# Optimization experiments

Hardware: AMD Instinct MI355X
Metric: run time of the kernel (lower is better)

Reference implementation:

```python
import jax, jax.numpy as jnp
import numpy as np

N_SRC = 50000
N_DST = 50000
E = 1600000
IN_DIM = 128
OUT_DIM = 128
EDGE_DIM = 64
NUM_HEADS = 4
HEAD_DIM = OUT_DIM // NUM_HEADS


def setup_inputs() -> dict:
    key = jax.random.key(0)
    ks = jax.random.split(key, 10)
    return {
        "h_src": jax.random.normal(ks[0], (N_SRC, IN_DIM), dtype=jnp.float32),
        "h_dst": jax.random.normal(ks[1], (N_DST, IN_DIM), dtype=jnp.float32),
        "edge_feat": jax.random.normal(ks[2], (E, EDGE_DIM), dtype=jnp.float32),
        "edge_index": jnp.stack([
            jax.random.randint(ks[3], (E,), 0, N_SRC),
            jax.random.randint(ks[4], (E,), 0, N_DST),
        ], axis=0).astype(jnp.int64) if False else jnp.stack([
            jax.random.randint(ks[3], (E,), 0, N_SRC),
            jax.random.randint(ks[4], (E,), 0, N_DST),
        ], axis=0),
        # weights stored [in, out]; y = x @ W (same math as torch Linear with W^T)
        "W_src": jax.random.normal(ks[5], (IN_DIM, OUT_DIM), dtype=jnp.float32) * 0.05,
        "W_dst": jax.random.normal(ks[6], (IN_DIM, OUT_DIM), dtype=jnp.float32) * 0.05,
        "W_edge": jax.random.normal(ks[7], (EDGE_DIM, OUT_DIM), dtype=jnp.float32) * 0.05,
        "a_src": jax.random.normal(ks[8], (NUM_HEADS, HEAD_DIM), dtype=jnp.float32) * 0.1,
        "a_dst": jax.random.normal(ks[9], (NUM_HEADS, HEAD_DIM), dtype=jnp.float32) * 0.1,
        "a_edge": jax.random.normal(jax.random.fold_in(key, 10), (NUM_HEADS, HEAD_DIM), dtype=jnp.float32) * 0.1,
    }


def reference(h_src, h_dst, edge_feat, edge_index, W_src, W_dst, W_edge, a_src, a_dst, a_edge):
    num_dst = h_dst.shape[0]
    src_idx, dst_idx = edge_index[0], edge_index[1]

    hs = (h_src @ W_src).reshape(-1, NUM_HEADS, HEAD_DIM)   # [N_src, H, D]
    hd = (h_dst @ W_dst).reshape(-1, NUM_HEADS, HEAD_DIM)   # [N_dst, H, D]
    he = (edge_feat @ W_edge).reshape(-1, NUM_HEADS, HEAD_DIM)  # [E, H, D]

    # per-node attention logit components, gathered to edges
    e_src_n = jnp.einsum('nhd,hd->nh', hs, a_src)  # [N_src, H]
    e_dst_n = jnp.einsum('nhd,hd->nh', hd, a_dst)  # [N_dst, H]
    e_edge = jnp.einsum('ehd,hd->eh', he, a_edge)  # [E, H]
    e = e_src_n[src_idx] + e_dst_n[dst_idx] + e_edge  # [E, H]
    e = jnp.where(e > 0, e, 0.2 * e)  # leaky_relu(0.2)

    # segmented softmax over edges grouped by destination node
    e_max = jax.ops.segment_max(e, dst_idx, num_segments=num_dst)  # [N_dst, H]
    e_max = jnp.where(jnp.isfinite(e_max), e_max, 0.0)  # empty segments
    e_exp = jnp.exp(e - e_max[dst_idx])  # [E, H]
    e_sum = jax.ops.segment_sum(e_exp, dst_idx, num_segments=num_dst)  # [N_dst, H]
    alpha = e_exp / (e_sum[dst_idx] + 1e-8)  # [E, H]

    # weighted scatter-aggregate of source features
    msg = alpha[..., None] * hs[src_idx]  # [E, H, D]
    out = jax.ops.segment_sum(msg, dst_idx, num_segments=num_dst)  # [N_dst, H, D]
    return out.reshape(num_dst, NUM_HEADS * HEAD_DIM)
```

## Files before the change

### kernel.cpp

```cpp
#include <hip/hip_runtime.h>

typedef _Float16 half_t;

#define N_SRCN 50000
#define N_DSTN 50000
#define NE     1600000
#define IN_DIM 128
#define OUT_DIMN 128
#define EDGE_DIMN 64
#define NHEAD  4
#define HDIM   32


__global__ __launch_bounds__(512) void k_combine(
    const float* __restrict__ Wsrc, const float* __restrict__ Wdst,
    const float* __restrict__ Wedge,
    const float* __restrict__ asrc, const float* __restrict__ adst,
    const float* __restrict__ aedge,
    float* __restrict__ c_src, float* __restrict__ c_dst,
    float* __restrict__ c_edgeH) {
    int t = threadIdx.x;
    int k = t >> 2, h = t & 3;
    float s1 = 0.f, s2 = 0.f;
    #pragma unroll
    for (int d = 0; d < HDIM; ++d) {
        s1 += Wsrc[k * OUT_DIMN + h * HDIM + d] * asrc[h * HDIM + d];
        s2 += Wdst[k * OUT_DIMN + h * HDIM + d] * adst[h * HDIM + d];
    }
    c_src[t] = s1;
    c_dst[t] = s2;
    if (t < EDGE_DIMN * NHEAD) {
        float s3 = 0.f;
        #pragma unroll
        for (int d = 0; d < HDIM; ++d)
            s3 += Wedge[k * OUT_DIMN + h * HDIM + d] * aedge[h * HDIM + d];
        c_edgeH[h * EDGE_DIMN + k] = s3;
    }
}

__global__ __launch_bounds__(256) void k_node_logits(
    const float* __restrict__ X, const float* __restrict__ c,
    float* __restrict__ outl, int N) {
    int row = blockIdx.x * 4 + (threadIdx.x >> 6);
    int l = threadIdx.x & 63;
    if (row >= N) return;
    float x0 = X[(size_t)row * IN_DIM + l];
    float x1 = X[(size_t)row * IN_DIM + 64 + l];
    #pragma unroll
    for (int h = 0; h < NHEAD; ++h) {
        float s = x0 * c[l * 4 + h] + x1 * c[(64 + l) * 4 + h];
        #pragma unroll
        for (int off = 32; off; off >>= 1) s += __shfl_xor(s, off, 64);
        if (l == h) outl[(size_t)row * 4 + h] = s;
    }
}

__global__ __launch_bounds__(256) void k_hist(
    const int* __restrict__ dstI, int* __restrict__ counts) {
    int e = blockIdx.x * 256 + threadIdx.x;
    if (e < NE) atomicAdd(&counts[dstI[e]], 1);
}

__global__ __launch_bounds__(1024) void k_scan(
    const int* __restrict__ cnt, int* __restrict__ offs, int* __restrict__ cur) {
    __shared__ int wbase[17];
    __shared__ int carry_s;
    int t = threadIdx.x;
    int lane = t & 63, w = t >> 6;
    if (t == 0) carry_s = 0;
    __syncthreads();
    for (int base = 0; base < N_DSTN; base += 4096) {
        int idx = base + t * 4;
        int4 c = make_int4(0, 0, 0, 0);
        if (idx < N_DSTN) c = *(const int4*)(cnt + idx);
        int s4 = c.x + c.y + c.z + c.w;
        int incl = s4;
        #pragma unroll
        for (int off = 1; off < 64; off <<= 1) {
            int v = __shfl_up(incl, off, 64);
            if (lane >= off) incl += v;
        }
        if (lane == 63) wbase[w] = incl;
        __syncthreads();
        if (t == 0) {
            int run = 0;
            #pragma unroll
            for (int q = 0; q < 16; ++q) { int v = wbase[q]; wbase[q] = run; run += v; }
            wbase[16] = run;
        }
        __syncthreads();
        int ebase = carry_s + wbase[w] + (incl - s4);
        if (idx < N_DSTN) {
            int4 o;
            int run = ebase;
            o.x = run; run += c.x;
            o.y = run; run += c.y;
            o.z = run; run += c.z;
            o.w = run; run += c.w;
            *(int4*)(offs + idx) = o;
            *(int4*)(cur + idx) = o;
        }
        __syncthreads();
        if (t == 0) carry_s += wbase[16];
        __syncthreads();
    }
    if (t == 0) offs[N_DSTN] = carry_s;
}

__global__ __launch_bounds__(256) void k_scatter(
    const int* __restrict__ dstI, int* __restrict__ cursor,
    int* __restrict__ perm) {
    int e = blockIdx.x * 256 + threadIdx.x;
    if (e < NE) {
        int d = dstI[e];
        int pos = atomicAdd(&cursor[d], 1);
        perm[pos] = e;
    }
}

__global__ __launch_bounds__(256) void k_gemm_half(
    const float* __restrict__ A, const float* __restrict__ W,
    half_t* __restrict__ C, int M, int c0) {
    __shared__ float As[64][68];
    __shared__ float Ws[64][68];
    int t = threadIdx.x;
    int tx = t & 15, ty = t >> 4;
    int rowbase = blockIdx.x * 64;
    float acc[4][4];
    #pragma unroll
    for (int i = 0; i < 4; ++i)
        #pragma unroll
        for (int j = 0; j < 4; ++j) acc[i][j] = 0.f;

    for (int kc = 0; kc < IN_DIM; kc += 64) {
        #pragma unroll
        for (int p = 0; p < 4; ++p) {
            int flat = p * 1024 + t * 4;
            int r = flat >> 6, ck = flat & 63;
            float4 v = make_float4(0.f, 0.f, 0.f, 0.f);
            if (rowbase + r < M)
                v = *(const float4*)(A + (size_t)(rowbase + r) * IN_DIM + kc + ck);
            *(float4*)(&As[r][ck]) = v;
        }
        #pragma unroll
        for (int p = 0; p < 4; ++p) {
            int flat = p * 1024 + t * 4;
            int kk = flat >> 6, col = flat & 63;
            *(float4*)(&Ws[kk][col]) =
                *(const float4*)(W + (size_t)(kc + kk) * OUT_DIMN + c0 + col);
        }
        __syncthreads();
        #pragma unroll
        for (int k = 0; k < 64; ++k) {
            float a[4], b[4];
            #pragma unroll
            for (int i = 0; i < 4; ++i) a[i] = As[ty * 4 + i][k];
            #pragma unroll
            for (int j = 0; j < 4; ++j) b[j] = Ws[k][tx + j * 16];
            #pragma unroll
            for (int i = 0; i < 4; ++i)
                #pragma unroll
                for (int j = 0; j < 4; ++j) acc[i][j] += a[i] * b[j];
        }
        __syncthreads();
    }
    #pragma unroll
    for (int i = 0; i < 4; ++i) {
        int row = rowbase + ty * 4 + i;
        if (row < M) {
            #pragma unroll
            for (int j = 0; j < 4; ++j)
                C[(size_t)row * 64 + tx + j * 16] = (half_t)acc[i][j];
        }
    }
}

__global__ __launch_bounds__(256) void k_gather(
    const int* __restrict__ offs, const int* __restrict__ perm,
    const int* __restrict__ srcI,
    const float* __restrict__ EF, const float* __restrict__ ceH,
    const float* __restrict__ esrc, const float* __restrict__ edstl,
    const half_t* __restrict__ hsH, float* __restrict__ out, int pass) {
    int d = blockIdx.x * 4 + (threadIdx.x >> 6);
    if (d >= N_DSTN) return;
    int l = threadIdx.x & 63;
    int g = l >> 5;
    int j = l & 31;
    int h = pass * 2 + g;
    float2 c2 = ((const float2*)(ceH + h * EDGE_DIMN))[j];
    float ed = edstl[(size_t)d * 4 + h];
    int start = offs[d], end = offs[d + 1];
    float acc = 0.f, den = 0.f;
    int eid = (start < end) ? perm[start] : 0;
    int si  = (start < end) ? srcI[eid] : 0;
    for (int i = start; i < end; ++i) {
        int eid_n = 0, si_n = 0;
        if (i + 1 < end) { eid_n = perm[i + 1]; si_n = srcI[eid_n]; }
        float2 v = ((const float2*)(EF + (size_t)eid * EDGE_DIMN))[j];
        float s = v.x * c2.x + v.y * c2.y;
        s += __shfl_xor(s, 1, 64);
        s += __shfl_xor(s, 2, 64);
        s += __shfl_xor(s, 4, 64);
        s += __shfl_xor(s, 8, 64);
        s += __shfl_xor(s, 16, 64);
        float z = esrc[(size_t)si * 4 + h] + ed + s;
        z = z > 0.f ? z : 0.2f * z;
        float ez = __expf(z);
        den += ez;
        acc += ez * (float)hsH[(size_t)si * 64 + l];
        eid = eid_n; si = si_n;
    }
    out[(size_t)d * OUT_DIMN + pass * 64 + l] = acc / (den + 1e-8f);
}

extern "C" void kernel_launch(void* const* d_in, const int* in_sizes, int n_in,
                              void* d_out, int out_size, void* d_ws, size_t ws_size,
                              hipStream_t stream) {
    const float* h_src     = (const float*)d_in[0];
    const float* h_dst     = (const float*)d_in[1];
    const float* edge_feat = (const float*)d_in[2];
    const int*   eidx      = (const int*)d_in[3];
    const float* Wsrc      = (const float*)d_in[4];
    const float* Wdst      = (const float*)d_in[5];
    const float* Wedge     = (const float*)d_in[6];
    const float* asrc      = (const float*)d_in[7];
    const float* adst      = (const float*)d_in[8];
    const float* aedge     = (const float*)d_in[9];
    float* out = (float*)d_out;

    char* W = (char*)d_ws;
    half_t* hsH    = (half_t*)(W + 0);
    int*   perm    = (int*)(W + 6400000);
    float* esrc    = (float*)(W + 12800000);
    float* edstl   = (float*)(W + 13600000);
    int*   offs    = (int*)(W + 14400000);
    int*   cursor  = (int*)(W + 14600016);
    int*   counts  = (int*)(W + 14800016);
    float* c_src   = (float*)(W + 15000016);
    float* c_dst   = (float*)(W + 15002064);
    float* c_edgeH = (float*)(W + 15004112);

    const int* srcI = eidx;
    const int* dstI = eidx + NE;

    hipMemsetAsync(counts, 0, N_DSTN * sizeof(int), stream);

    k_combine<<<1, 512, 0, stream>>>(Wsrc, Wdst, Wedge, asrc, adst, aedge,
                                     c_src, c_dst, c_edgeH);
    k_node_logits<<<(N_SRCN + 3) / 4, 256, 0, stream>>>(h_src, c_src, esrc, N_SRCN);
    k_node_logits<<<(N_DSTN + 3) / 4, 256, 0, stream>>>(h_dst, c_dst, edstl, N_DSTN);

    k_hist<<<(NE + 255) / 256, 256, 0, stream>>>(dstI, counts);
    k_scan<<<1, 1024, 0, stream>>>(counts, offs, cursor);
    k_scatter<<<(NE + 255) / 256, 256, 0, stream>>>(dstI, cursor, perm);

    k_gemm_half<<<(N_SRCN + 63) / 64, 256, 0, stream>>>(h_src, Wsrc, hsH, N_SRCN, 0);
    k_gather<<<(N_DSTN + 3) / 4, 256, 0, stream>>>(offs, perm, srcI, edge_feat,
                                                   c_edgeH, esrc, edstl, hsH, out, 0);
    k_gemm_half<<<(N_SRCN + 63) / 64, 256, 0, stream>>>(h_src, Wsrc, hsH, N_SRCN, 64);
    k_gather<<<(N_DSTN + 3) / 4, 256, 0, stream>>>(offs, perm, srcI, edge_feat,
                                                   c_edgeH, esrc, edstl, hsH, out, 1);
}
```

Measured before the change: 1.466 ms.

## Software-pipeline edge gather, vectorize node logits, parallelize scan, use DPP reductions

The gather kernel now keeps a multi-stage software pipeline that prefetches perm, srcI, edge features, source logits and half features several edges ahead. The edge-logit dot product uses float4 loads with a 16-lane DPP row reduction instead of a 32-lane shuffle tree. Node logits are computed with 16 threads per row using float4 loads and a transposed coefficient layout. The single-block serial scan is replaced by a three-kernel block-parallel scan. Together these aim to hide gather latency and remove the serial scan bottleneck, at the cost of more registers and two extra launches.

```diff
diff --git a/kernel.cpp b/kernel.cpp
--- a/kernel.cpp
+++ b/kernel.cpp
@@ -11,13 +11,23 @@
 #define NHEAD  4
 #define HDIM   32
 
+#define ROR_ADD(x, CTRL) ((x) + __int_as_float(__builtin_amdgcn_update_dpp( \
+    0, __float_as_int(x), (CTRL), 0xF, 0xF, false)))
+__device__ __forceinline__ float sum16(float s) {
+    s = ROR_ADD(s, 0x121);
+    s = ROR_ADD(s, 0x122);
+    s = ROR_ADD(s, 0x124);
+    s = ROR_ADD(s, 0x128);
+    return s;
+}
+
 
 __global__ __launch_bounds__(512) void k_combine(
     const float* __restrict__ Wsrc, const float* __restrict__ Wdst,
     const float* __restrict__ Wedge,
     const float* __restrict__ asrc, const float* __restrict__ adst,
     const float* __restrict__ aedge,
-    float* __restrict__ c_src, float* __restrict__ c_dst,
+    float* __restrict__ c_srcH, float* __restrict__ c_dstH,
     float* __restrict__ c_edgeH) {
     int t = threadIdx.x;
     int k = t >> 2, h = t & 3;
@@ -27,8 +37,8 @@
         s1 += Wsrc[k * OUT_DIMN + h * HDIM + d] * asrc[h * HDIM + d];
         s2 += Wdst[k * OUT_DIMN + h * HDIM + d] * adst[h * HDIM + d];
     }
-    c_src[t] = s1;
-    c_dst[t] = s2;
+    c_srcH[h * IN_DIM + k] = s1;
+    c_dstH[h * IN_DIM + k] = s2;
     if (t < EDGE_DIMN * NHEAD) {
         float s3 = 0.f;
         #pragma unroll
@@ -39,20 +49,29 @@
 }
 
 __global__ __launch_bounds__(256) void k_node_logits(
-    const float* __restrict__ X, const float* __restrict__ c,
+    const float* __restrict__ X, const float* __restrict__ cH,
     float* __restrict__ outl, int N) {
-    int row = blockIdx.x * 4 + (threadIdx.x >> 6);
-    int l = threadIdx.x & 63;
+    int t = threadIdx.x;
+    int row = blockIdx.x * 16 + (t >> 4);
+    int q = t & 15;
     if (row >= N) return;
-    float x0 = X[(size_t)row * IN_DIM + l];
-    float x1 = X[(size_t)row * IN_DIM + 64 + l];
-    #pragma unroll
-    for (int h = 0; h < NHEAD; ++h) {
-        float s = x0 * c[l * 4 + h] + x1 * c[(64 + l) * 4 + h];
-        #pragma unroll
-        for (int off = 32; off; off >>= 1) s += __shfl_xor(s, off, 64);
-        if (l == h) outl[(size_t)row * 4 + h] = s;
-    }
+    const float4* X4 = (const float4*)X;
+    const float4* C4 = (const float4*)cH;
+    float4 xa = X4[(size_t)row * 32 + q];
+    float4 xb = X4[(size_t)row * 32 + 16 + q];
+    float s0, s1, s2, s3;
+    #pragma unroll
+    for (int h = 0; h < 4; ++h) {
+        float4 ca = C4[h * 32 + q];
+        float4 cb = C4[h * 32 + 16 + q];
+        float v = xa.x * ca.x + xa.y * ca.y + xa.z * ca.z + xa.w * ca.w
+                + xb.x * cb.x + xb.y * cb.y + xb.z * cb.z + xb.w * cb.w;
+        v = sum16(v);
+        if (h == 0) s0 = v; else if (h == 1) s1 = v;
+        else if (h == 2) s2 = v; else s3 = v;
+    }
+    float v = (q == 0) ? s0 : (q == 1) ? s1 : (q == 2) ? s2 : s3;
+    if (q < 4) outl[(size_t)row * 4 + q] = v;
 }
 
 __global__ __launch_bounds__(256) void k_hist(
@@ -61,50 +80,53 @@
     if (e < NE) atomicAdd(&counts[dstI[e]], 1);
 }
 
-__global__ __launch_bounds__(1024) void k_scan(
-    const int* __restrict__ cnt, int* __restrict__ offs, int* __restrict__ cur) {
-    __shared__ int wbase[17];
-    __shared__ int carry_s;
-    int t = threadIdx.x;
+__global__ __launch_bounds__(1024) void k_scan_part(
+    const int* __restrict__ cnt, int* __restrict__ offs, int* __restrict__ bsum) {
+    __shared__ int wsum[16];
+    int t = threadIdx.x, b = blockIdx.x;
+    int idx = b * 1024 + t;
     int lane = t & 63, w = t >> 6;
-    if (t == 0) carry_s = 0;
+    int c = (idx < N_DSTN) ? cnt[idx] : 0;
+    int incl = c;
+    #pragma unroll
+    for (int off = 1; off < 64; off <<= 1) {
+        int v = __shfl_up(incl, off, 64);
+        if (lane >= off) incl += v;
+    }
+    if (lane == 63) wsum[w] = incl;
     __syncthreads();
-    for (int base = 0; base < N_DSTN; base += 4096) {
-        int idx = base + t * 4;
-        int4 c = make_int4(0, 0, 0, 0);
-        if (idx < N_DSTN) c = *(const int4*)(cnt + idx);
-        int s4 = c.x + c.y + c.z + c.w;
-        int incl = s4;
-        #pragma unroll
-        for (int off = 1; off < 64; off <<= 1) {
-            int v = __shfl_up(incl, off, 64);
-            if (lane >= off) incl += v;
-        }
-        if (lane == 63) wbase[w] = incl;
-        __syncthreads();
-        if (t == 0) {
-            int run = 0;
-            #pragma unroll
-            for (int q = 0; q < 16; ++q) { int v = wbase[q]; wbase[q] = run; run += v; }
-            wbase[16] = run;
-        }
-        __syncthreads();
-        int ebase = carry_s + wbase[w] + (incl - s4);
-        if (idx < N_DSTN) {
-            int4 o;
-            int run = ebase;
-            o.x = run; run += c.x;
-            o.y = run; run += c.y;
-            o.z = run; run += c.z;
-            o.w = run; run += c.w;
-            *(int4*)(offs + idx) = o;
-            *(int4*)(cur + idx) = o;
-        }
-        __syncthreads();
-        if (t == 0) carry_s += wbase[16];
-        __syncthreads();
-    }
-    if (t == 0) offs[N_DSTN] = carry_s;
+    if (t == 0) {
+        int run = 0;
+        #pragma unroll
+        for (int qq = 0; qq < 16; ++qq) { int v = wsum[qq]; wsum[qq] = run; run += v; }
+        bsum[b] = run;
+    }
+    __syncthreads();
+    if (idx < N_DSTN) offs[idx] = wsum[w] + incl - c;
+}
+
+__global__ __launch_bounds__(64) void k_scan_mid(
+    int* __restrict__ bsum, int* __restrict__ offs, int nb) {
+    int l = threadIdx.x;
+    int v = (l < nb) ? bsum[l] : 0;
+    int incl = v;
+    #pragma unroll
+    for (int off = 1; off < 64; off <<= 1) {
+        int u = __shfl_up(incl, off, 64);
+        if (l >= off) incl += u;
+    }
+    if (l < nb) bsum[l] = incl - v;
+    if (l == 63) offs[N_DSTN] = incl;
+}
+
+__global__ __launch_bounds__(1024) void k_scan_add(
+    int* __restrict__ offs, int* __restrict__ cursor, const int* __restrict__ bsum) {
+    int idx = blockIdx.x * 1024 + threadIdx.x;
+    if (idx < N_DSTN) {
+        int v = offs[idx] + bsum[blockIdx.x];
+        offs[idx] = v;
+        cursor[idx] = v;
+    }
 }
 
 __global__ __launch_bounds__(256) void k_scatter(
@@ -184,32 +206,54 @@
     int d = blockIdx.x * 4 + (threadIdx.x >> 6);
     if (d >= N_DSTN) return;
     int l = threadIdx.x & 63;
-    int g = l >> 5;
-    int j = l & 31;
-    int h = pass * 2 + g;
-    float2 c2 = ((const float2*)(ceH + h * EDGE_DIMN))[j];
+    int q = l & 15;
+    int h = pass * 2 + (l >> 5);
+    int start = offs[d], end = offs[d + 1];
+    int n = end - start;
+    if (n <= 0) { out[(size_t)d * OUT_DIMN + pass * 64 + l] = 0.f; return; }
+
+    const float4* EF4 = (const float4*)EF;
+    float4 c4 = ((const float4*)ceH)[h * 16 + q];
     float ed = edstl[(size_t)d * 4 + h];
-    int start = offs[d], end = offs[d + 1];
+    int end1 = end - 1;
+    #define PCLAMP(i) perm[(start + (i) < end) ? (start + (i)) : end1]
+
+    int a0 = PCLAMP(0), a1 = PCLAMP(1), a2 = PCLAMP(2);
+    int e3 = PCLAMP(3), e4 = PCLAMP(4);
+    int b0 = srcI[a0], b1 = srcI[a1], b2 = srcI[a2];
+    int s3 = srcI[e3];
+    float4 v0 = EF4[(size_t)a0 * 16 + q];
+    float4 v1 = EF4[(size_t)a1 * 16 + q];
+    float4 v2 = EF4[(size_t)a2 * 16 + q];
+    float f0 = esrc[(size_t)b0 * 4 + h];
+    float f1 = esrc[(size_t)b1 * 4 + h];
+    float f2 = esrc[(size_t)b2 * 4 + h];
+    half_t g0 = hsH[(size_t)b0 * 64 + l];
+    half_t g1 = hsH[(size_t)b1 * 64 + l];
+    half_t g2 = hsH[(size_t)b2 * 64 + l];
+
     float acc = 0.f, den = 0.f;
-    int eid = (start < end) ? perm[start] : 0;
-    int si  = (start < end) ? srcI[eid] : 0;
-    for (int i = start; i < end; ++i) {
-        int eid_n = 0, si_n = 0;
-        if (i + 1 < end) { eid_n = perm[i + 1]; si_n = srcI[eid_n]; }
-        float2 v = ((const float2*)(EF + (size_t)eid * EDGE_DIMN))[j];
-        float s = v.x * c2.x + v.y * c2.y;
-        s += __shfl_xor(s, 1, 64);
-        s += __shfl_xor(s, 2, 64);
-        s += __shfl_xor(s, 4, 64);
-        s += __shfl_xor(s, 8, 64);
-        s += __shfl_xor(s, 16, 64);
-        float z = esrc[(size_t)si * 4 + h] + ed + s;
+    for (int i = 0; i < n; ++i) {
+        int e5 = PCLAMP(i + 5);
+        int s4 = srcI[e4];
+        float4 vN = EF4[(size_t)e3 * 16 + q];
+        float  fN = esrc[(size_t)s3 * 4 + h];
+        half_t gN = hsH[(size_t)s3 * 64 + l];
+
+        float s = v0.x * c4.x + v0.y * c4.y + v0.z * c4.z + v0.w * c4.w;
+        s = sum16(s);
+        float z = f0 + ed + s;
         z = z > 0.f ? z : 0.2f * z;
         float ez = __expf(z);
         den += ez;
-        acc += ez * (float)hsH[(size_t)si * 64 + l];
-        eid = eid_n; si = si_n;
-    }
+        acc += ez * (float)g0;
+
+        v0 = v1; v1 = v2; v2 = vN;
+        f0 = f1; f1 = f2; f2 = fN;
+        g0 = g1; g1 = g2; g2 = gN;
+        e3 = e4; e4 = e5; s3 = s4;
+    }
+    #undef PCLAMP
     out[(size_t)d * OUT_DIMN + pass * 64 + l] = acc / (den + 1e-8f);
 }
 
@@ -236,22 +280,27 @@
     int*   offs    = (int*)(W + 14400000);
     int*   cursor  = (int*)(W + 14600016);
     int*   counts  = (int*)(W + 14800016);
-    float* c_src   = (float*)(W + 15000016);
-    float* c_dst   = (float*)(W + 15002064);
+    float* c_srcH  = (float*)(W + 15000016);
+    float* c_dstH  = (float*)(W + 15002064);
     float* c_edgeH = (float*)(W + 15004112);
+    int*   bsum    = (int*)(W + 15005136);
 
     const int* srcI = eidx;
     const int* dstI = eidx + NE;
 
+    const int NB_SCAN = (N_DSTN + 1023) / 1024;
+
     hipMemsetAsync(counts, 0, N_DSTN * sizeof(int), stream);
 
     k_combine<<<1, 512, 0, stream>>>(Wsrc, Wdst, Wedge, asrc, adst, aedge,
-                                     c_src, c_dst, c_edgeH);
-    k_node_logits<<<(N_SRCN + 3) / 4, 256, 0, stream>>>(h_src, c_src, esrc, N_SRCN);
-    k_node_logits<<<(N_DSTN + 3) / 4, 256, 0, stream>>>(h_dst, c_dst, edstl, N_DSTN);
+                                     c_srcH, c_dstH, c_edgeH);
+    k_node_logits<<<(N_SRCN + 15) / 16, 256, 0, stream>>>(h_src, c_srcH, esrc, N_SRCN);
+    k_node_logits<<<(N_DSTN + 15) / 16, 256, 0, stream>>>(h_dst, c_dstH, edstl, N_DSTN);
 
     k_hist<<<(NE + 255) / 256, 256, 0, stream>>>(dstI, counts);
-    k_scan<<<1, 1024, 0, stream>>>(counts, offs, cursor);
+    k_scan_part<<<NB_SCAN, 1024, 0, stream>>>(counts, offs, bsum);
+    k_scan_mid<<<1, 64, 0, stream>>>(bsum, offs, NB_SCAN);
+    k_scan_add<<<NB_SCAN, 1024, 0, stream>>>(offs, cursor, bsum);
     k_scatter<<<(NE + 255) / 256, 256, 0, stream>>>(dstI, cursor, perm);
 
     k_gemm_half<<<(N_SRCN + 63) / 64, 256, 0, stream>>>(h_src, Wsrc, hsH, N_SRCN, 0);
```

New measurement: 1.405 ms. 4.2% less time.
